# Kernel optimization log

Hardware: AMD Instinct MI355X
Metric: run time of the kernel (lower is better)

## Reference

```python
import jax, jax.numpy as jnp
import numpy as np

B, X_DIM, Y_DIM, HIDDEN = 512, 768, 128, 1024
H2 = HIDDEN // 2


def setup_inputs() -> dict:
    key = jax.random.key(0)
    ks = jax.random.split(key, 10)
    s_in = 1.0 / np.sqrt(X_DIM)
    s_h = 1.0 / np.sqrt(H2)
    return {
        "x_samples": jax.random.normal(ks[0], (B, X_DIM), jnp.float32),
        "y_samples": jax.random.normal(ks[1], (B, Y_DIM), jnp.float32),
        "w1_mu": jax.random.uniform(ks[2], (X_DIM, H2), jnp.float32, -s_in, s_in),
        "b1_mu": jax.random.uniform(ks[3], (H2,), jnp.float32, -s_in, s_in),
        "w2_mu": jax.random.uniform(ks[4], (H2, Y_DIM), jnp.float32, -s_h, s_h),
        "b2_mu": jax.random.uniform(ks[5], (Y_DIM,), jnp.float32, -s_h, s_h),
        "w1_lv": jax.random.uniform(ks[6], (X_DIM, H2), jnp.float32, -s_in, s_in),
        "b1_lv": jax.random.uniform(ks[7], (H2,), jnp.float32, -s_in, s_in),
        "w2_lv": jax.random.uniform(ks[8], (H2, Y_DIM), jnp.float32, -s_h, s_h),
        "b2_lv": jax.random.uniform(ks[9], (Y_DIM,), jnp.float32, -s_h, s_h),
    }


def reference(x_samples, y_samples, w1_mu, b1_mu, w2_mu, b2_mu,
              w1_lv, b1_lv, w2_lv, b2_lv):
    batch = y_samples.shape[0]
    # p_mu / p_logvar MLP heads
    mu = jax.nn.relu(x_samples @ w1_mu + b1_mu) @ w2_mu + b2_mu          # [B, Y]
    logvar = jnp.tanh(jax.nn.relu(x_samples @ w1_lv + b1_lv) @ w2_lv + b2_lv)  # [B, Y]

    inv_var = jnp.exp(-logvar)
    # positive: diagonal Gaussian log-prob of y_i under p(.|x_i), up to const
    positive = (-0.5 * (mu - y_samples) ** 2 * inv_var - 0.5 * logvar).sum(-1)  # [B]

    # pairwise log-probs: row i = params from x_i, col j = sample y_j
    mu_1 = mu[:, None, :]            # [B, 1, Y]
    lv_1 = logvar[:, None, :]        # [B, 1, Y]
    y_1 = y_samples[None, :, :]      # [1, B, Y]
    all_probs = (-0.5 * (y_1 - mu_1) ** 2 * jnp.exp(-lv_1) - 0.5 * lv_1).sum(-1)  # [B, B]

    # Faithful replication of the torch broadcasting: diag_mask is [B, B, 1],
    # so all_probs + diag_mask broadcasts to [B, B, B], then logsumexp over dim 0.
    diag_mask = (jnp.eye(batch, dtype=all_probs.dtype) * -20.0)[:, :, None]  # [B, B, 1]
    logits = all_probs + diag_mask                                           # [B, B, B]
    negative = jax.scipy.special.logsumexp(logits, axis=0) - jnp.log(batch - 1.0)  # [B, B]

    return (positive - negative).mean()
```

## Files before the change

### kernel.cpp

```cpp
#include <hip/hip_runtime.h>
#include <math.h>

#define BSZ   512
#define XD    768
#define YD    128
#define H2D   512


__global__ __launch_bounds__(256, 2) void layer1_kernel(
    const float* __restrict__ x,
    const float* __restrict__ w1_mu, const float* __restrict__ w1_lv,
    float* __restrict__ p1)
{
    __shared__ float As[16][68];
    __shared__ float Bs[16][68];

    const int t      = threadIdx.x;
    const int branch = blockIdx.z >> 2;
    const int ks     = blockIdx.z & 3;
    const float* __restrict__ W = branch ? w1_lv : w1_mu;
    float* __restrict__ out = p1 + (size_t)blockIdx.z * (BSZ * H2D);

    const int m0 = blockIdx.x * 64;
    const int n0 = blockIdx.y * 64;
    const int tx = t & 15;
    const int ty = t >> 4;

    const int am  = t >> 2;
    const int akq = (t & 3) * 4;
    const int bkk = t >> 4;
    const int bnq = (t & 15) * 4;

    const int kbase = ks * 192;
    float acc[4][4] = {};

    float4 ap = *(const float4*)&x[(m0 + am) * XD + kbase + akq];
    float4 bp = *(const float4*)&W[(kbase + bkk) * H2D + n0 + bnq];

    for (int kt = 0; kt < 192; kt += 16) {
        __syncthreads();
        As[akq + 0][am] = ap.x; As[akq + 1][am] = ap.y;
        As[akq + 2][am] = ap.z; As[akq + 3][am] = ap.w;
        *(float4*)&Bs[bkk][bnq] = bp;
        __syncthreads();
        if (kt + 16 < 192) {
            const int kn = kbase + kt + 16;
            ap = *(const float4*)&x[(m0 + am) * XD + kn + akq];
            bp = *(const float4*)&W[(kn + bkk) * H2D + n0 + bnq];
        }
        #pragma unroll
        for (int k = 0; k < 16; ++k) {
            const float4 a4 = *(const float4*)&As[k][ty * 4];
            const float4 b4 = *(const float4*)&Bs[k][tx * 4];
            acc[0][0] += a4.x*b4.x; acc[0][1] += a4.x*b4.y; acc[0][2] += a4.x*b4.z; acc[0][3] += a4.x*b4.w;
            acc[1][0] += a4.y*b4.x; acc[1][1] += a4.y*b4.y; acc[1][2] += a4.y*b4.z; acc[1][3] += a4.y*b4.w;
            acc[2][0] += a4.z*b4.x; acc[2][1] += a4.z*b4.y; acc[2][2] += a4.z*b4.z; acc[2][3] += a4.z*b4.w;
            acc[3][0] += a4.w*b4.x; acc[3][1] += a4.w*b4.y; acc[3][2] += a4.w*b4.z; acc[3][3] += a4.w*b4.w;
        }
    }

    #pragma unroll
    for (int i = 0; i < 4; ++i) {
        const float4 o = make_float4(acc[i][0], acc[i][1], acc[i][2], acc[i][3]);
        *(float4*)&out[(m0 + ty * 4 + i) * H2D + n0 + tx * 4] = o;
    }
}

__global__ __launch_bounds__(256, 2) void layer2_kernel(
    const float* __restrict__ p1,
    const float* __restrict__ b1_mu, const float* __restrict__ b1_lv,
    const float* __restrict__ w2_mu, const float* __restrict__ w2_lv,
    const float* __restrict__ y,
    float* __restrict__ p2,
    double* __restrict__ Sy, double* __restrict__ Sy2,
    double* __restrict__ accum, unsigned int* __restrict__ counter)
{
    __shared__ float Hc[32][68];
    const int t = threadIdx.x;

    if (blockIdx.z == 16) {
        const int id = blockIdx.x;
        const int dl = t & 7;
        const int g  = t >> 3;
        const int d  = id * 8 + dl;
        float s = 0.f, s2 = 0.f;
        #pragma unroll
        for (int i = g * 16; i < g * 16 + 16; ++i) {
            const float v = y[i * YD + d];
            s += v; s2 += v * v;
        }
        float* shs  = &Hc[0][0];
        float* shs2 = &Hc[0][0] + 512;
        shs[t] = s; shs2[t] = s2;
        __syncthreads();
        if (t < 8) {
            double S = 0.0, S2 = 0.0;
            #pragma unroll
            for (int gg = 0; gg < 32; ++gg) {
                S += (double)shs[gg * 8 + t]; S2 += (double)shs2[gg * 8 + t];
            }
            Sy[id * 8 + t] = S; Sy2[id * 8 + t] = S2;
        } else if (id == 0 && t == 8)  { accum[0] = 0.0; }
        else if (id == 0 && t == 9)  { accum[1] = 0.0; }
        else if (id == 0 && t == 10) { *counter = 0u; }
        return;
    }

    const int branch = blockIdx.z >> 3;
    const int ks     = blockIdx.z & 7;
    const float* __restrict__ q  = p1 + (size_t)(branch * 4) * (BSZ * H2D);
    const float* __restrict__ b1 = branch ? b1_lv : b1_mu;
    const float* __restrict__ W  = branch ? w2_lv : w2_mu;
    float* __restrict__ out = p2 + (size_t)blockIdx.z * (BSZ * YD);

    const int m0   = blockIdx.x * 32;
    const int kb   = ks * 64;
    const int lane = t & 63;
    const int wave = t >> 6;

    {
        const int row  = t >> 3;
        const int kq   = (t & 7) * 8;
        const int base = (m0 + row) * H2D + kb + kq;
        float4 h0 = *(const float4*)&b1[kb + kq];
        float4 h1 = *(const float4*)&b1[kb + kq + 4];
        #pragma unroll
        for (int s = 0; s < 4; ++s) {
            const float4 v0 = *(const float4*)&q[(size_t)s * (BSZ * H2D) + base];
            const float4 v1 = *(const float4*)&q[(size_t)s * (BSZ * H2D) + base + 4];
            h0.x += v0.x; h0.y += v0.y; h0.z += v0.z; h0.w += v0.w;
            h1.x += v1.x; h1.y += v1.y; h1.z += v1.z; h1.w += v1.w;
        }
        h0.x = fmaxf(h0.x, 0.f); h0.y = fmaxf(h0.y, 0.f);
        h0.z = fmaxf(h0.z, 0.f); h0.w = fmaxf(h0.w, 0.f);
        h1.x = fmaxf(h1.x, 0.f); h1.y = fmaxf(h1.y, 0.f);
        h1.z = fmaxf(h1.z, 0.f); h1.w = fmaxf(h1.w, 0.f);
        *(float4*)&Hc[row][kq]     = h0;
        *(float4*)&Hc[row][kq + 4] = h1;
    }
    __syncthreads();

    const int wm0 = wave * 8;
    float acc0[8] = {}, acc1[8] = {};
    #pragma unroll
    for (int half = 0; half < 2; ++half) {
        const int kh = kb + half * 32;
        float br0[32], br1[32];
        #pragma unroll
        for (int k = 0; k < 32; ++k) {
            br0[k] = W[(kh + k) * YD + lane];
            br1[k] = W[(kh + k) * YD + 64 + lane];
        }
        #pragma unroll
        for (int m = 0; m < 8; ++m) {
            const float* hrow = &Hc[wm0 + m][half * 32];
            #pragma unroll
            for (int qd = 0; qd < 8; ++qd) {
                const float4 a4 = *(const float4*)&hrow[qd * 4];
                acc0[m] += a4.x * br0[qd * 4 + 0]; acc1[m] += a4.x * br1[qd * 4 + 0];
                acc0[m] += a4.y * br0[qd * 4 + 1]; acc1[m] += a4.y * br1[qd * 4 + 1];
                acc0[m] += a4.z * br0[qd * 4 + 2]; acc1[m] += a4.z * br1[qd * 4 + 2];
                acc0[m] += a4.w * br0[qd * 4 + 3]; acc1[m] += a4.w * br1[qd * 4 + 3];
            }
        }
    }

    #pragma unroll
    for (int m = 0; m < 8; ++m) {
        const int row = (m0 + wm0 + m) * YD;
        out[row + lane]      = acc0[m];
        out[row + 64 + lane] = acc1[m];
    }
}

__global__ __launch_bounds__(256) void reduce_kernel(
    const float* __restrict__ p2, const float* __restrict__ y,
    const float* __restrict__ b2_mu, const float* __restrict__ b2_lv,
    const double* __restrict__ Sy, const double* __restrict__ Sy2,
    double* __restrict__ accum, unsigned int* __restrict__ counter,
    float* __restrict__ outp)
{
    const int NE = BSZ * YD;
    const int e  = blockIdx.x * 256 + threadIdx.x;
    const int d  = e & (YD - 1);

    float mu = b2_mu[d];
    float lp = b2_lv[d];
    #pragma unroll
    for (int s = 0; s < 8; ++s) {
        mu += p2[s * NE + e];
        lp += p2[(8 + s) * NE + e];
    }
    const float lv = tanhf(lp);
    const float iv = expf(-lv);
    const float dm = mu - y[e];

    double pos = -0.5 * (double)dm * (double)dm * (double)iv - 0.5 * (double)lv;
    double ap  = (double)iv * (-0.5 * Sy2[d] + (double)mu * Sy[d]
                               - 256.0 * (double)mu * (double)mu)
               - 256.0 * (double)lv;

    #pragma unroll
    for (int off = 32; off > 0; off >>= 1) {
        pos += __shfl_down(pos, off);
        ap  += __shfl_down(ap, off);
    }
    __shared__ double sp[4];
    __shared__ double sa[4];
    const int lane = threadIdx.x & 63;
    const int wv   = threadIdx.x >> 6;
    if (lane == 0) { sp[wv] = pos; sa[wv] = ap; }
    __syncthreads();
    if (threadIdx.x == 0) {
        atomicAdd(&accum[0], sp[0] + sp[1] + sp[2] + sp[3]);
        atomicAdd(&accum[1], sa[0] + sa[1] + sa[2] + sa[3]);
        __threadfence();
        const unsigned int old = atomicAdd(counter, 1u);
        if (old == 255u) {
            const double P = atomicAdd(&accum[0], 0.0);
            const double A = atomicAdd(&accum[1], 0.0);
            const double C = log1p(exp(-20.0) / 511.0);
            outp[0] = (float)(P / 512.0 - A / 262144.0 - C);
        }
    }
}

extern "C" void kernel_launch(void* const* d_in, const int* in_sizes, int n_in,
                              void* d_out, int out_size, void* d_ws, size_t ws_size,
                              hipStream_t stream) {
    const float* x     = (const float*)d_in[0];
    const float* y     = (const float*)d_in[1];
    const float* w1_mu = (const float*)d_in[2];
    const float* b1_mu = (const float*)d_in[3];
    const float* w2_mu = (const float*)d_in[4];
    const float* b2_mu = (const float*)d_in[5];
    const float* w1_lv = (const float*)d_in[6];
    const float* b1_lv = (const float*)d_in[7];
    const float* w2_lv = (const float*)d_in[8];
    const float* b2_lv = (const float*)d_in[9];

    char* ws = (char*)d_ws;
    float*  p1 = (float*)(ws);
    float*  p2 = (float*)(ws + (size_t)8 * BSZ * H2D * 4);
    double* Sy = (double*)(ws + (size_t)8 * BSZ * H2D * 4
                              + (size_t)16 * BSZ * YD * 4);
    double* Sy2 = Sy + YD;
    double* accum = Sy2 + YD;
    unsigned int* counter = (unsigned int*)(accum + 2);

    layer1_kernel<<<dim3(8, 8, 8), 256, 0, stream>>>(x, w1_mu, w1_lv, p1);
    layer2_kernel<<<dim3(16, 1, 17), 256, 0, stream>>>(
        p1, b1_mu, b1_lv, w2_mu, w2_lv, y, p2, Sy, Sy2, accum, counter);
    reduce_kernel<<<256, 256, 0, stream>>>(
        p2, y, b2_mu, b2_lv, Sy, Sy2, accum, counter, (float*)d_out);
}
```

Baseline: 111.5 us.

## Enlarge layer1 GEMM tiles to 128x128 with 8x8 micro-tiles and 8-way split-K

Layer1 now uses 128x128 output tiles with a 32-deep K slice and an 8x8 per-thread register micro-tile, replacing 64x64 tiles with 4x4 micro-tiles. Split-K goes from 4 to 8 partitions so the grid still holds 256 blocks. The aim is more FMA work per shared-memory load and higher arithmetic intensity. In exchange, layer2 must read and sum 8 partial buffers instead of 4, the workspace doubles, and register pressure rises with the 64 accumulators per thread, which may lower occupancy.

```diff
diff --git a/kernel.cpp b/kernel.cpp
--- a/kernel.cpp
+++ b/kernel.cpp
@@ -7,62 +7,86 @@
 #define H2D   512
 
 
-__global__ __launch_bounds__(256, 2) void layer1_kernel(
+__global__ __launch_bounds__(256) void layer1_kernel(
     const float* __restrict__ x,
     const float* __restrict__ w1_mu, const float* __restrict__ w1_lv,
     float* __restrict__ p1)
 {
-    __shared__ float As[16][68];
-    __shared__ float Bs[16][68];
+    __shared__ float As[32][132];
+    __shared__ float Bs[32][132];
 
     const int t      = threadIdx.x;
-    const int branch = blockIdx.z >> 2;
-    const int ks     = blockIdx.z & 3;
+    const int branch = blockIdx.z >> 3;
+    const int ks     = blockIdx.z & 7;
     const float* __restrict__ W = branch ? w1_lv : w1_mu;
     float* __restrict__ out = p1 + (size_t)blockIdx.z * (BSZ * H2D);
 
-    const int m0 = blockIdx.x * 64;
-    const int n0 = blockIdx.y * 64;
+    const int m0 = blockIdx.x * 128;
+    const int n0 = blockIdx.y * 128;
     const int tx = t & 15;
     const int ty = t >> 4;
 
-    const int am  = t >> 2;
-    const int akq = (t & 3) * 4;
-    const int bkk = t >> 4;
-    const int bnq = (t & 15) * 4;
-
-    const int kbase = ks * 192;
-    float acc[4][4] = {};
-
-    float4 ap = *(const float4*)&x[(m0 + am) * XD + kbase + akq];
-    float4 bp = *(const float4*)&W[(kbase + bkk) * H2D + n0 + bnq];
-
-    for (int kt = 0; kt < 192; kt += 16) {
+    const int am  = t & 127;
+    const int akb = (t >> 7) * 16;
+    const int bn  = (t & 31) * 4;
+    const int bk  = t >> 5;
+
+    const int kbase = ks * 96;
+    float acc[8][8] = {};
+
+    float4 apf[4], bpf[4];
+    {
+        const float* xr = &x[(m0 + am) * XD + kbase + akb];
+        #pragma unroll
+        for (int j = 0; j < 4; ++j) apf[j] = *(const float4*)&xr[j * 4];
+        #pragma unroll
+        for (int j = 0; j < 4; ++j)
+            bpf[j] = *(const float4*)&W[(kbase + bk + 8 * j) * H2D + n0 + bn];
+    }
+
+    for (int kt = 0; kt < 96; kt += 32) {
         __syncthreads();
-        As[akq + 0][am] = ap.x; As[akq + 1][am] = ap.y;
-        As[akq + 2][am] = ap.z; As[akq + 3][am] = ap.w;
-        *(float4*)&Bs[bkk][bnq] = bp;
+        #pragma unroll
+        for (int j = 0; j < 4; ++j) {
+            As[akb + 4 * j + 0][am] = apf[j].x;
+            As[akb + 4 * j + 1][am] = apf[j].y;
+            As[akb + 4 * j + 2][am] = apf[j].z;
+            As[akb + 4 * j + 3][am] = apf[j].w;
+            *(float4*)&Bs[bk + 8 * j][bn] = bpf[j];
+        }
         __syncthreads();
-        if (kt + 16 < 192) {
-            const int kn = kbase + kt + 16;
-            ap = *(const float4*)&x[(m0 + am) * XD + kn + akq];
-            bp = *(const float4*)&W[(kn + bkk) * H2D + n0 + bnq];
-        }
-        #pragma unroll
-        for (int k = 0; k < 16; ++k) {
-            const float4 a4 = *(const float4*)&As[k][ty * 4];
-            const float4 b4 = *(const float4*)&Bs[k][tx * 4];
-            acc[0][0] += a4.x*b4.x; acc[0][1] += a4.x*b4.y; acc[0][2] += a4.x*b4.z; acc[0][3] += a4.x*b4.w;
-            acc[1][0] += a4.y*b4.x; acc[1][1] += a4.y*b4.y; acc[1][2] += a4.y*b4.z; acc[1][3] += a4.y*b4.w;
-            acc[2][0] += a4.z*b4.x; acc[2][1] += a4.z*b4.y; acc[2][2] += a4.z*b4.z; acc[2][3] += a4.z*b4.w;
-            acc[3][0] += a4.w*b4.x; acc[3][1] += a4.w*b4.y; acc[3][2] += a4.w*b4.z; acc[3][3] += a4.w*b4.w;
-        }
-    }
-
-    #pragma unroll
-    for (int i = 0; i < 4; ++i) {
-        const float4 o = make_float4(acc[i][0], acc[i][1], acc[i][2], acc[i][3]);
-        *(float4*)&out[(m0 + ty * 4 + i) * H2D + n0 + tx * 4] = o;
+        if (kt + 32 < 96) {
+            const int kn = kbase + kt + 32;
+            const float* xr = &x[(m0 + am) * XD + kn + akb];
+            #pragma unroll
+            for (int j = 0; j < 4; ++j) apf[j] = *(const float4*)&xr[j * 4];
+            #pragma unroll
+            for (int j = 0; j < 4; ++j)
+                bpf[j] = *(const float4*)&W[(kn + bk + 8 * j) * H2D + n0 + bn];
+        }
+        #pragma unroll
+        for (int k = 0; k < 32; ++k) {
+            const float4 a0 = *(const float4*)&As[k][ty * 4];
+            const float4 a1 = *(const float4*)&As[k][64 + ty * 4];
+            const float4 b0 = *(const float4*)&Bs[k][tx * 4];
+            const float4 b1 = *(const float4*)&Bs[k][64 + tx * 4];
+            const float av[8] = {a0.x, a0.y, a0.z, a0.w, a1.x, a1.y, a1.z, a1.w};
+            const float bv[8] = {b0.x, b0.y, b0.z, b0.w, b1.x, b1.y, b1.z, b1.w};
+            #pragma unroll
+            for (int i = 0; i < 8; ++i)
+                #pragma unroll
+                for (int j = 0; j < 8; ++j)
+                    acc[i][j] += av[i] * bv[j];
+        }
+    }
+
+    #pragma unroll
+    for (int i = 0; i < 8; ++i) {
+        const int row = m0 + (i >> 2) * 64 + ty * 4 + (i & 3);
+        *(float4*)&out[row * H2D + n0 + tx * 4] =
+            make_float4(acc[i][0], acc[i][1], acc[i][2], acc[i][3]);
+        *(float4*)&out[row * H2D + n0 + 64 + tx * 4] =
+            make_float4(acc[i][4], acc[i][5], acc[i][6], acc[i][7]);
     }
 }
 
@@ -108,7 +132,7 @@
 
     const int branch = blockIdx.z >> 3;
     const int ks     = blockIdx.z & 7;
-    const float* __restrict__ q  = p1 + (size_t)(branch * 4) * (BSZ * H2D);
+    const float* __restrict__ q  = p1 + (size_t)(branch * 8) * (BSZ * H2D);
     const float* __restrict__ b1 = branch ? b1_lv : b1_mu;
     const float* __restrict__ W  = branch ? w2_lv : w2_mu;
     float* __restrict__ out = p2 + (size_t)blockIdx.z * (BSZ * YD);
@@ -125,7 +149,7 @@
         float4 h0 = *(const float4*)&b1[kb + kq];
         float4 h1 = *(const float4*)&b1[kb + kq + 4];
         #pragma unroll
-        for (int s = 0; s < 4; ++s) {
+        for (int s = 0; s < 8; ++s) {
             const float4 v0 = *(const float4*)&q[(size_t)s * (BSZ * H2D) + base];
             const float4 v1 = *(const float4*)&q[(size_t)s * (BSZ * H2D) + base + 4];
             h0.x += v0.x; h0.y += v0.y; h0.z += v0.z; h0.w += v0.w;
@@ -241,14 +265,14 @@
 
     char* ws = (char*)d_ws;
     float*  p1 = (float*)(ws);
-    float*  p2 = (float*)(ws + (size_t)8 * BSZ * H2D * 4);
-    double* Sy = (double*)(ws + (size_t)8 * BSZ * H2D * 4
+    float*  p2 = (float*)(ws + (size_t)16 * BSZ * H2D * 4);
+    double* Sy = (double*)(ws + (size_t)16 * BSZ * H2D * 4
                               + (size_t)16 * BSZ * YD * 4);
     double* Sy2 = Sy + YD;
     double* accum = Sy2 + YD;
     unsigned int* counter = (unsigned int*)(accum + 2);
 
-    layer1_kernel<<<dim3(8, 8, 8), 256, 0, stream>>>(x, w1_mu, w1_lv, p1);
+    layer1_kernel<<<dim3(4, 4, 16), 256, 0, stream>>>(x, w1_mu, w1_lv, p1);
     layer2_kernel<<<dim3(16, 1, 17), 256, 0, stream>>>(
         p1, b1_mu, b1_lv, w2_mu, w2_lv, y, p2, Sy, Sy2, accum, counter);
     reduce_kernel<<<256, 256, 0, stream>>>(
```

After: 114.1 us. 1.02x slower.
